# Kernel tuning notes

Measured on AMD Instinct MI355X. Metric: run time of the kernel, lower is better.

## Reference

```python
import jax, jax.numpy as jnp
import numpy as np

DILATIONS = (48, 76, 96, 111, 124, 135, 144, 152)


def setup_inputs() -> dict:
    key = jax.random.key(0)
    kx, kw, kb = jax.random.split(key, 3)
    B_, C_IN, H, Wd = 8, 64, 128, 512
    C_OUT = 64
    x = jax.random.normal(kx, (B_, C_IN, H, Wd), dtype=jnp.float32)
    # stacked weights for 8 parallel branches: [branch, out_ch, in_ch, kh=1, kw=3]
    W = jax.random.normal(kw, (8, C_OUT, C_IN, 1, 3), dtype=jnp.float32) * 0.05
    B = jax.random.normal(kb, (8, C_OUT), dtype=jnp.float32) * 0.05
    return {"x": x, "W": W, "B": B}


def _dilated_conv(x, w, d):
    # 'same' padding for kernel (1,3) with dilation (1,d): pad d on each side of width
    return jax.lax.conv_general_dilated(
        x, w,
        window_strides=(1, 1),
        padding=[(0, 0), (d, d)],
        rhs_dilation=(1, d),
        dimension_numbers=("NCHW", "OIHW", "NCHW"),
    )


def reference(x, W, B):
    out = None
    for i, d in enumerate(DILATIONS):  # fixed small structural loop over branches
        y = _dilated_conv(x, W[i], d) + B[i][None, :, None, None]
        out = y if out is None else out + y
    return jax.nn.relu(out)
```

## Files before the change

kernel.cpp:

```cpp
#include <hip/hip_runtime.h>
#include <hip/hip_bf16.h>
#include <stdint.h>

typedef float  f32x4 __attribute__((ext_vector_type(4)));
typedef short  s16x8 __attribute__((ext_vector_type(8)));

#define NB    8
#define CIN   64
#define COUT  64
#define HH    128
#define WW    512
#define NTAP  17
#define PADW  152
#define XROW  816
#define BUFB  (XROW * 64)
#define HW    (HH * WW)

__global__ __launch_bounds__(256) void prep_wfrag(
        const float* __restrict__ W, const float* __restrict__ Bv,
        __hip_bfloat16* __restrict__ wf, float* __restrict__ bsum) {
    int idx = blockIdx.x * 256 + threadIdx.x;
    if (idx < NTAP * 2 * 4 * 64 * 8) {
        int j  = idx & 7;
        int l  = (idx >> 3) & 63;
        int m  = (idx >> 9) & 3;
        int pp = (idx >> 11) & 1;
        int t  = idx >> 12;
        int ci = pp * 32 + 8 * (l >> 4) + j;
        int co = 16 * m + (l & 15);
        float v;
        if (t == 0) {
            v = 0.f;
            #pragma unroll
            for (int i = 0; i < NB; ++i) v += W[((i * COUT + co) * CIN + ci) * 3 + 1];
        } else if (t <= 8) {
            v = W[(((t - 1) * COUT + co) * CIN + ci) * 3 + 0];
        } else {
            v = W[(((t - 9) * COUT + co) * CIN + ci) * 3 + 2];
        }
        wf[idx] = __float2bfloat16(v);
    }
    if (idx < COUT) {
        float s = 0.f;
        #pragma unroll
        for (int i = 0; i < NB; ++i) s += Bv[i * COUT + idx];
        bsum[idx] = s;
    }
}

static constexpr int OFFS[NTAP] = {0, -48, -76, -96, -111, -124, -135, -144, -152,
                                      48,  76,  96,  111,  124,  135,  144,  152};

#define SB __builtin_amdgcn_sched_barrier(0)

#define LOADAF(AF, T0, CNT)                                                    \
    _Pragma("unroll")                                                          \
    for (int i = 0; i < (CNT); ++i)                                            \
        _Pragma("unroll")                                                      \
        for (int mm = 0; mm < 2; ++mm)                                         \
            AF[i][mm] = *reinterpret_cast<const s16x8*>(                       \
                wbase + ((T0) + i) * 8192 + (2 * mg + mm) * 1024);

#define COMPTAPS(AF, T0, CNT)                                                  \
    _Pragma("unroll")                                                          \
    for (int i = 0; i < (CNT); ++i) {                                          \
        const int t      = (T0) + i;                                           \
        const int ldsrow = rowb + OFFS[t];                                     \
        const int slot   = lhi ^ ((ldsrow >> 1) & 3);                          \
        const char* bbase = rb + ldsrow * 64 + slot * 16;                      \
        s16x8 bfr[8];                                                          \
        _Pragma("unroll")                                                      \
        for (int n = 0; n < 8; ++n)                                            \
            bfr[n] = *reinterpret_cast<const s16x8*>(bbase + n * 1024);        \
        _Pragma("unroll")                                                      \
        for (int mm = 0; mm < 2; ++mm)                                         \
            _Pragma("unroll")                                                  \
            for (int n = 0; n < 8; ++n)                                        \
                acc[mm][n] = __builtin_amdgcn_mfma_f32_16x16x32_bf16(          \
                    AF[i][mm], bfr[n], acc[mm][n], 0, 0, 0);                   \
    }

__global__ __launch_bounds__(512, 2) void hdc_mfma(
        const float* __restrict__ x, const __hip_bfloat16* __restrict__ wf,
        const float* __restrict__ bsum, float* __restrict__ out) {
    extern __shared__ __align__(16) char smem[];

    const int tid  = threadIdx.x;
    const int wv   = tid >> 6;
    const int lane = tid & 63;
    const int l15  = lane & 15;
    const int lhi  = lane >> 4;
    const int mg   = wv >> 2;
    const int ws   = wv & 3;
    const int c    = tid >> 7;
    const int wl   = tid & 127;
    const int bh0  = blockIdx.x * 4;
    const int wlo  = ws * 128;
    const int rowb = PADW + wlo + l15;

    f32x4 acc[2][8];
    #pragma unroll
    for (int mm = 0; mm < 2; ++mm) {
        f32x4 bi = *reinterpret_cast<const f32x4*>(
            bsum + mg * 32 + 16 * mm + 4 * lhi);
        #pragma unroll
        for (int n = 0; n < 8; ++n) acc[mm][n] = bi;
    }

    {
        const int4 z{0, 0, 0, 0};
        #pragma unroll
        for (int bb = 0; bb < 2; ++bb) {
            int4* base = reinterpret_cast<int4*>(smem + bb * BUFB);
            for (int f = tid; f < 608; f += 512) {
                base[f] = z;
                base[2656 + f] = z;
            }
        }
    }

    float4 xv[8];

    auto SLOAD = [&](int u) {
        const int r = bh0 + (u >> 1);
        const int b = r >> 7, h = r & 127;
        const float* src = x +
            (((size_t)(b * CIN + (u & 1) * 32 + c * 8) * HH + h) * WW) + wl * 4;
        #pragma unroll
        for (int j = 0; j < 8; ++j)
            xv[j] = *reinterpret_cast<const float4*>(src + j * HW);
    };
    auto SWRITE = [&](int u) {
        char* dst = smem + (u & 1) * BUFB;
        #pragma unroll
        for (int k = 0; k < 4; ++k) {
            const int row  = PADW + wl * 4 + k;
            const int slot = c ^ ((row >> 1) & 3);
            union { __hip_bfloat16 hs[8]; int4 iv; } pk;
            #pragma unroll
            for (int j = 0; j < 8; ++j)
                pk.hs[j] = __float2bfloat16(((const float*)&xv[j])[k]);
            *reinterpret_cast<int4*>(dst + row * 64 + slot * 16) = pk.iv;
        }
    };

    SLOAD(0);
    asm volatile("s_waitcnt vmcnt(0)" ::: "memory");
    SB;
    SWRITE(0);
    __syncthreads();

    for (int u = 0; u < 8; ++u) {
        const char* wbase = (const char*)wf + (u & 1) * 4096 + lane * 16;
        const char* rb    = smem + (u & 1) * BUFB;

        s16x8 af0[4][2], af1[4][2], af2[4][2], af3[5][2];

        LOADAF(af0, 0, 4)  SB;
        COMPTAPS(af0, 0, 4) SB;
        LOADAF(af1, 4, 4)  SB;
        COMPTAPS(af1, 4, 4) SB;
        LOADAF(af2, 8, 4)  SB;
        COMPTAPS(af2, 8, 4) SB;
        LOADAF(af3, 12, 5) SB;
        if (u < 7) SLOAD(u + 1);
        SB;
        COMPTAPS(af3, 12, 5) SB;

        if (u & 1) {
            const int r = bh0 + (u >> 1);
            const int b = r >> 7, h = r & 127;
            float* obase = out +
                (((size_t)b * COUT + mg * 32 + 4 * lhi) * HH + h) * WW + wlo + l15;
            #pragma unroll
            for (int mm = 0; mm < 2; ++mm)
                #pragma unroll
                for (int n = 0; n < 8; ++n)
                    #pragma unroll
                    for (int rr = 0; rr < 4; ++rr) {
                        float v = acc[mm][n][rr];
                        obase[(size_t)(16 * mm + rr) * HW + 16 * n] =
                            v > 0.f ? v : 0.f;
                    }
            #pragma unroll
            for (int mm = 0; mm < 2; ++mm) {
                f32x4 bi = *reinterpret_cast<const f32x4*>(
                    bsum + mg * 32 + 16 * mm + 4 * lhi);
                #pragma unroll
                for (int n = 0; n < 8; ++n) acc[mm][n] = bi;
            }
        }

        if (u < 7) {
            asm volatile("s_waitcnt vmcnt(0)" ::: "memory");
            SB;
            SWRITE(u + 1);
        }

        asm volatile("s_waitcnt lgkmcnt(0)" ::: "memory");
        SB;
        __builtin_amdgcn_s_barrier();
    }
}

#define CI_STAGE 16

__global__ void prep_weff_fb(const float* __restrict__ W, const float* __restrict__ Bv,
                             float* __restrict__ weff, float* __restrict__ bsum) {
    int idx = blockIdx.x * 256 + threadIdx.x;
    if (idx < CIN * NTAP * COUT) {
        int co = idx & 63;
        int t  = (idx >> 6) % NTAP;
        int ci = idx / (NTAP * COUT);
        float v;
        if (t == 0) {
            v = 0.f;
            #pragma unroll
            for (int i = 0; i < NB; ++i) v += W[(((i * COUT + co) * CIN + ci) * 3) + 1];
        } else if (t <= 8) {
            v = W[((((t - 1) * COUT + co) * CIN + ci) * 3) + 0];
        } else {
            v = W[((((t - 9) * COUT + co) * CIN + ci) * 3) + 2];
        }
        weff[(ci * NTAP + t) * COUT + co] = v;
    }
    if (idx < COUT) {
        float s = 0.f;
        #pragma unroll
        for (int i = 0; i < NB; ++i) s += Bv[i * COUT + idx];
        bsum[idx] = s;
    }
}

__global__ __launch_bounds__(256, 2) void hdc_fb(
        const float* __restrict__ x, const float* __restrict__ weff,
        const float* __restrict__ bsum, float* __restrict__ out) {
    __shared__ float xsf[CI_STAGE][XROW];
    const int bh  = blockIdx.x;
    const int b   = bh >> 7;
    const int h   = bh & (HH - 1);
    const int tid = threadIdx.x;
    const int cg  = tid >> 5;
    const int wl  = tid & 31;
    float acc[8][16];
    #pragma unroll
    for (int j = 0; j < 8; ++j) {
        const float bj = bsum[cg * 8 + j];
        #pragma unroll
        for (int i = 0; i < 16; ++i) acc[j][i] = bj;
    }
    const float* xrowbase = x + ((size_t)(b * CIN) * HH + h) * WW;
    for (int s = 0; s < CIN / CI_STAGE; ++s) {
        __syncthreads();
        for (int f = tid; f < CI_STAGE * PADW; f += 256) {
            int r = f / PADW, cc = f - r * PADW;
            xsf[r][cc] = 0.f;
            xsf[r][PADW + WW + cc] = 0.f;
        }
        #pragma unroll
        for (int j = 0; j < 8; ++j) {
            int flat = j * 256 + tid;
            int r = flat >> 7, c4 = flat & 127;
            const float4 v = *reinterpret_cast<const float4*>(
                xrowbase + (size_t)(s * CI_STAGE + r) * HW + c4 * 4);
            *reinterpret_cast<float4*>(&xsf[r][PADW + c4 * 4]) = v;
        }
        __syncthreads();
        for (int r = 0; r < CI_STAGE; ++r) {
            const int ci = s * CI_STAGE + r;
            const float* wrow = weff + (size_t)(ci * NTAP) * COUT + cg * 8;
            const float* xr   = &xsf[r][PADW + wl];
            #pragma unroll
            for (int t = 0; t < NTAP; ++t) {
                const float4 w0 = *reinterpret_cast<const float4*>(wrow + t * COUT);
                const float4 w1 = *reinterpret_cast<const float4*>(wrow + t * COUT + 4);
                float xvv[16];
                #pragma unroll
                for (int i = 0; i < 16; ++i) xvv[i] = xr[OFFS[t] + 32 * i];
                const float wv2[8] = {w0.x, w0.y, w0.z, w0.w, w1.x, w1.y, w1.z, w1.w};
                #pragma unroll
                for (int j = 0; j < 8; ++j)
                    #pragma unroll
                    for (int i = 0; i < 16; ++i)
                        acc[j][i] = fmaf(wv2[j], xvv[i], acc[j][i]);
            }
        }
    }
    float* outbase = out + (((size_t)b * COUT + cg * 8) * HH + h) * WW + wl;
    #pragma unroll
    for (int j = 0; j < 8; ++j)
        #pragma unroll
        for (int i = 0; i < 16; ++i) {
            float v = acc[j][i];
            outbase[(size_t)j * HW + 32 * i] = v > 0.f ? v : 0.f;
        }
}


extern "C" void kernel_launch(void* const* d_in, const int* in_sizes, int n_in,
                              void* d_out, int out_size, void* d_ws, size_t ws_size,
                              hipStream_t stream) {
    const float* x  = (const float*)d_in[0];
    const float* W  = (const float*)d_in[1];
    const float* Bv = (const float*)d_in[2];
    float* out = (float*)d_out;

    const size_t need = 139264 + 256;

    if (ws_size >= need) {
        __hip_bfloat16* wf = (__hip_bfloat16*)d_ws;
        float* bsum = (float*)((char*)d_ws + 139264);
        prep_wfrag<<<272, 256, 0, stream>>>(W, Bv, wf, bsum);
        (void)hipFuncSetAttribute((const void*)hdc_mfma,
            hipFuncAttributeMaxDynamicSharedMemorySize, 2 * BUFB);
        hdc_mfma<<<256, 512, 2 * BUFB, stream>>>(x, wf, bsum, out);
    } else {
        float* weff = (float*)d_ws;
        float* bsum = weff + (size_t)CIN * NTAP * COUT;
        prep_weff_fb<<<(CIN * NTAP * COUT + 255) / 256, 256, 0, stream>>>(W, Bv, weff, bsum);
        hdc_fb<<<NB * HH, 256, 0, stream>>>(x, weff, bsum, out);
    }
}
```

Before: 80.61 us.

## Double-buffer weight fragment loads and stagger tap order across wave groups

Replaces the sequential load-then-compute of four tap groups with a ping-pong scheme over six groups of three taps. The weight fragments for the next group are fetched while the current group's MFMAs run. The next row's global loads are issued earlier in the unit. The two M-groups of waves start at different tap offsets, which spreads out LDS bank and global weight traffic. This is meant to hide weight-load latency behind MFMA work, at the cost of code size and a possible rise in register pressure under launch bounds (512,2).

New measurement: 78.77 us, median of 3. 2.3% less time.

```diff
diff --git a/kernel.cpp b/kernel.cpp
--- a/kernel.cpp
+++ b/kernel.cpp
@@ -80,6 +80,25 @@
                     AF[i][mm], bfr[n], acc[mm][n], 0, 0, 0);                   \
     }
 
+#define UNIT_SCHED(U, B1,C1, B2,C2, B3,C3, B4,C4, B5,C5, B6,C6)                \
+    {                                                                          \
+        s16x8 afA[3][2], afB[3][2];                                            \
+        LOADAF(afA, B1, C1)   SB;                                              \
+        LOADAF(afB, B2, C2)   SB;                                              \
+        if ((U) < 7) SLOAD((U) + 1);                                           \
+        SB;                                                                    \
+        COMPTAPS(afA, B1, C1) SB;                                              \
+        LOADAF(afA, B3, C3)   SB;                                              \
+        COMPTAPS(afB, B2, C2) SB;                                              \
+        LOADAF(afB, B4, C4)   SB;                                              \
+        COMPTAPS(afA, B3, C3) SB;                                              \
+        LOADAF(afA, B5, C5)   SB;                                              \
+        COMPTAPS(afB, B4, C4) SB;                                              \
+        LOADAF(afB, B6, C6)   SB;                                              \
+        COMPTAPS(afA, B5, C5) SB;                                              \
+        COMPTAPS(afB, B6, C6) SB;                                              \
+    }
+
 __global__ __launch_bounds__(512, 2) void hdc_mfma(
         const float* __restrict__ x, const __hip_bfloat16* __restrict__ wf,
         const float* __restrict__ bsum, float* __restrict__ out) {
@@ -154,18 +173,11 @@
         const char* wbase = (const char*)wf + (u & 1) * 4096 + lane * 16;
         const char* rb    = smem + (u & 1) * BUFB;
 
-        s16x8 af0[4][2], af1[4][2], af2[4][2], af3[5][2];
-
-        LOADAF(af0, 0, 4)  SB;
-        COMPTAPS(af0, 0, 4) SB;
-        LOADAF(af1, 4, 4)  SB;
-        COMPTAPS(af1, 4, 4) SB;
-        LOADAF(af2, 8, 4)  SB;
-        COMPTAPS(af2, 8, 4) SB;
-        LOADAF(af3, 12, 5) SB;
-        if (u < 7) SLOAD(u + 1);
-        SB;
-        COMPTAPS(af3, 12, 5) SB;
+        if (mg == 0) {
+            UNIT_SCHED(u, 0,3, 3,3, 6,3, 9,3, 12,3, 15,2)
+        } else {
+            UNIT_SCHED(u, 9,3, 12,3, 15,2, 0,3, 3,3, 6,3)
+        }
 
         if (u & 1) {
             const int r = bh0 + (u >> 1);
```
